# Performance work log

Hardware: AMD Instinct MI355X
Metric: run time of the kernel (lower is better)

The kernel has to match this reference:

```python
import jax, jax.numpy as jnp
import numpy as np

B, T, C, H = 2, 2048, 1024, 4
D = C // H
STRIDES = [1, 3, 7, 13]  # spiral_strides[:n_head]
SCALE = 1.0 / float(np.sqrt(D))


def _build_mask():
    """Static [H, T, T] bool mask: spiral positions intersected with causal.
    Replicates: positions = set((i+offset)%T for offset in range(-T//2, T//2, stride)),
    then keep only p <= i."""
    m = np.zeros((H, T, T), dtype=bool)
    i = np.arange(T)
    causal = (np.arange(T)[None, :] <= i[:, None])
    for h in range(H):
        s = STRIDES[h % len(STRIDES)]
        off = np.arange(-(T // 2), T // 2, s)
        pos = (i[:, None] + off[None, :]) % T  # [T, n_off]
        mh = np.zeros((T, T), dtype=bool)
        mh[np.repeat(i, len(off)), pos.ravel()] = True  # set semantics (dupes ok)
        m[h] = mh & causal
    return jnp.asarray(m)

MASK = _build_mask()  # [H, T, T]


def setup_inputs() -> dict:
    ks = jax.random.split(jax.random.key(0), 4)
    s = 0.02
    return {
        "x": jax.random.normal(ks[0], (B, T, C), jnp.float32),
        "Wqk": jax.random.normal(ks[1], (C, C), jnp.float32) * s,
        "bqk": jnp.zeros((C,), jnp.float32),
        "Wv": jax.random.normal(ks[2], (C, C), jnp.float32) * s,
        "bv": jnp.zeros((C,), jnp.float32),
        "Wo": jax.random.normal(ks[3], (C, C), jnp.float32) * s,
        "bo": jnp.zeros((C,), jnp.float32),
    }


def reference(x, Wqk, bqk, Wv, bv, Wo, bo):
    qk = x @ Wqk.T + bqk                                   # [B,T,C]; q == k in source
    q = qk.reshape(B, T, H, D).transpose(0, 2, 1, 3)       # [B,H,T,D]
    v = (x @ Wv.T + bv).reshape(B, T, H, D).transpose(0, 2, 1, 3)
    scores = jnp.einsum('bhid,bhjd->bhij', q, q) * SCALE   # [B,H,T,T]
    NEG = jnp.float32(-1e30)
    logits = jnp.where(MASK[None], scores, NEG)
    w = jax.nn.softmax(logits, axis=-1)
    # Rows with no causal spiral position stay all-zero (matches torch scatter behavior)
    w = jnp.where(MASK[None], w, jnp.float32(0.0))
    out = jnp.einsum('bhij,bhjd->bhid', w, v)              # [B,H,T,D]
    out = out.transpose(0, 2, 1, 3).reshape(B, T, C)
    return out @ Wo.T + bo
```

## Files before the change

### kernel.cpp

```cpp
#include <hip/hip_runtime.h>
#include <cstdint>
#include <cstddef>

typedef unsigned short u16;
typedef uint32_t u32;
typedef __bf16 bf16x8 __attribute__((ext_vector_type(8)));
typedef float f32x4 __attribute__((ext_vector_type(4)));
typedef float f32x16 __attribute__((ext_vector_type(16)));

typedef __attribute__((address_space(1))) void gvoid;
typedef __attribute__((address_space(3))) void lvoid;

__device__ __forceinline__ void g2l16(const void* g, void* l) {
    __builtin_amdgcn_global_load_lds((gvoid*)g, (lvoid*)l, 16, 0, 0);
}

__device__ __forceinline__ u16 f2bf(float f) {
    union { float f; uint32_t u; } v;
    v.f = f;
    uint32_t r = (v.u + 0x7FFFu + ((v.u >> 16) & 1u)) >> 16;
    return (u16)r;
}

__device__ const int T_h[24]  = {0, 1,1,1, 2,2,2,2,2,2,2, 3,3,3,3,3,3,3,3,3,3,3,3,3};
__device__ const int T_g[24]  = {0, 0,1,2, 0,1,2,3,4,5,6, 0,1,2,3,4,5,6,7,8,9,10,11,12};
__device__ const int T_qt[24] = {0, 64,86,108, 130,140,150,160,170,180,190,
                                 200,205,210,215,220,225,230,235,240,245,250,255,260};
__device__ const int T_LQ[24] = {2048, 683,683,682, 293,293,293,293,292,292,292,
                                 158,158,158,158,158,158,158,157,157,157,157,157,157};
__device__ const int T_ktB[24]= {0, 64,86,108, 140,150,160,170,180,190,130,
                                 245,250,255,260,200,205,210,215,220,225,230,235,240};
__device__ const int T_LkB[24]= {2048, 683,683,682, 293,293,293,292,292,292,293,
                                 157,157,157,157,158,158,158,158,158,158,158,157,157};
__device__ const int T_cB[24] = {1, -341,-341,-341, -146,-146,-146,-146,-146,-146,-145,
                                 -79,-79,-79,-79,-78,-78,-78,-78,-78,-78,-78,-78,-78};
__device__ const int T_ktA[24]= {0, 108,64,86, 180,190,130,140,150,160,170,
                                 215,220,225,230,235,240,245,250,255,260,200,205,210};
__device__ const int T_LkA[24]= {0, 682,683,683, 292,292,293,293,293,293,292,
                                 158,158,158,158,157,157,157,157,157,157,158,158,158};
__device__ const int T_cA[24] = {0, -342,-341,-341, -147,-147,-146,-146,-146,-146,-146,
                                 -79,-79,-79,-79,-79,-79,-79,-79,-79,-79,-78,-78,-78};
__device__ const int T_dA[24] = {0, 0,1,1, 0,0,1,1,1,1,1, 0,0,0,0,0,0,0,0,0,0,1,1,1};
__device__ const int T_nc[24] = {16, 6,6,6, 3,3,3,3,3,3,3, 2,2,2,2,2,2,2,2,2,2,2,2,2};

__device__ __forceinline__ void col_geom(int p, int c, int& ntB, int& tA0, int& nt) {
    const int LQ = T_LQ[p];
    const int Mc = c << 7;
    int mmax = Mc + 128; if (mmax > LQ) mmax = LQ; mmax -= 1;
    int jB = mmax + T_cB[p];
    if (jB < 0) jB = 0;
    if (jB > T_LkB[p]) jB = T_LkB[p];
    ntB = (jB + 31) >> 5;
    int jlo = Mc + T_cA[p]; if (jlo < 0) jlo = 0;
    int jhi = mmax + T_dA[p];
    if (jhi > T_LkA[p]) jhi = T_LkA[p];
    tA0 = jlo >> 5;
    int ntA = 0;
    if (jhi > jlo) ntA = ((jhi + 31) >> 5) - tA0;
    nt = ntB + ntA;
}

__device__ __forceinline__ u16* partO_addr(u16* lo, u16* hi, int slot) {
    return (slot < 128) ? (lo + (size_t)slot * 32768) : (hi + (size_t)(slot - 128) * 32768);
}
__device__ __forceinline__ const u16* partO_addr_c(const u16* lo, const u16* hi, int slot) {
    return (slot < 128) ? (lo + (size_t)slot * 32768) : (hi + (size_t)(slot - 128) * 32768);
}

__global__ __launch_bounds__(256)
void cvt_kernel(const float* __restrict__ x, const float* __restrict__ wqk,
                const float* __restrict__ wv, const float* __restrict__ wo,
                u16* __restrict__ out) {
    int i = (blockIdx.x * 256 + threadIdx.x) * 4;
    const float* src;
    int off;
    if (i < 4194304)      { src = x;   off = 0; }
    else if (i < 5242880) { src = wqk; off = 4194304; }
    else if (i < 6291456) { src = wv;  off = 5242880; }
    else                  { src = wo;  off = 6291456; }
    float4 v = *(const float4*)(src + (i - off));
    ushort4 o;
    o.x = f2bf(v.x); o.y = f2bf(v.y); o.z = f2bf(v.z); o.w = f2bf(v.w);
    *(ushort4*)(out + i) = o;
}

__global__ __launch_bounds__(256, 3)
void gemm_qkv(const u16* __restrict__ A, const u16* __restrict__ Bq, const u16* __restrict__ Bv,
              const float* __restrict__ bq, const float* __restrict__ bv,
              u16* __restrict__ qkb, u16* __restrict__ vb) {
    __shared__ __align__(16) u16 As[2][4096], Bqs[2][2048], Bvs[2][2048];
    const int bid = blockIdx.x;
    const int m0 = (bid >> 4) * 128;
    const int n0 = (bid & 15) * 64;
    const int t = threadIdx.x;
    const int lane = t & 63;
    const int wid = t >> 6;
    const int wr = wid >> 1, wc = wid & 1;
    const int l15 = lane & 15, l4 = lane >> 4;

    f32x4 aq[4][2] = {}, av[4][2] = {};

    auto stage = [&](int buf, int kt) {
        const int kbase = kt * 32;
#pragma unroll
        for (int c2 = 0; c2 < 2; ++c2) {
            const int pp = c2 * 4096 + t * 16;
            g2l16(A + (size_t)(m0 + (pp >> 6)) * 1024 + kbase + ((pp & 63) >> 1), (char*)As[buf] + pp);
        }
        const int pb = t * 16;
        const int rb = pb >> 6, kb = (pb & 63) >> 1;
        g2l16(Bq + (size_t)(n0 + rb) * 1024 + kbase + kb, (char*)Bqs[buf] + pb);
        g2l16(Bv + (size_t)(n0 + rb) * 1024 + kbase + kb, (char*)Bvs[buf] + pb);
    };

    stage(0, 0);
    asm volatile("s_waitcnt vmcnt(0)" ::: "memory");
    __syncthreads();

    int cur = 0;
    for (int kt = 0; kt < 32; ++kt) {
        if (kt + 1 < 32) stage(cur ^ 1, kt + 1);
        bf16x8 af[4], bfq[2], bfv[2];
#pragma unroll
        for (int mi = 0; mi < 4; ++mi)
            af[mi] = *(const bf16x8*)((const char*)As[cur] + (wr * 64 + mi * 16 + l15) * 64 + l4 * 16);
#pragma unroll
        for (int ni = 0; ni < 2; ++ni) {
            bfq[ni] = *(const bf16x8*)((const char*)Bqs[cur] + (wc * 32 + ni * 16 + l15) * 64 + l4 * 16);
            bfv[ni] = *(const bf16x8*)((const char*)Bvs[cur] + (wc * 32 + ni * 16 + l15) * 64 + l4 * 16);
        }
        __builtin_amdgcn_s_setprio(1);
#pragma unroll
        for (int mi = 0; mi < 4; ++mi)
#pragma unroll
            for (int ni = 0; ni < 2; ++ni) {
                aq[mi][ni] = __builtin_amdgcn_mfma_f32_16x16x32_bf16(af[mi], bfq[ni], aq[mi][ni], 0, 0, 0);
                av[mi][ni] = __builtin_amdgcn_mfma_f32_16x16x32_bf16(af[mi], bfv[ni], av[mi][ni], 0, 0, 0);
            }
        __builtin_amdgcn_s_setprio(0);
        asm volatile("s_waitcnt vmcnt(0)" ::: "memory");
        __syncthreads();
        cur ^= 1;
    }

    const int mbase = m0 + wr * 64 + l4 * 4;
    const int nbase = n0 + wc * 32 + l15;
#pragma unroll
    for (int ni = 0; ni < 2; ++ni) {
        const int n = nbase + ni * 16;
        const float bq_ = bq[n];
        const float bv_ = bv[n];
#pragma unroll
        for (int mi = 0; mi < 4; ++mi) {
            const int mrow = mbase + mi * 16;
#pragma unroll
            for (int r = 0; r < 4; ++r) {
                qkb[(size_t)(mrow + r) * 1024 + n] = f2bf(aq[mi][ni][r] + bq_);
                vb [(size_t)(mrow + r) * 1024 + n] = f2bf(av[mi][ni][r] + bv_);
            }
        }
    }
}

__device__ __forceinline__ void tile_decode(int tt, int& h, int& cls, int& jt, int& LK) {
    if (tt < 64)       { h = 0; cls = 0;               jt = tt;              LK = 2048; }
    else if (tt < 130) { h = 1; cls = (tt - 64) / 22;  jt = (tt - 64) % 22;  LK = (cls < 2) ? 683 : 682; }
    else if (tt < 200) { h = 2; cls = (tt - 130) / 10; jt = (tt - 130) % 10; LK = (cls < 4) ? 293 : 292; }
    else               { h = 3; cls = (tt - 200) / 5;  jt = (tt - 200) % 5;  LK = (cls < 7) ? 158 : 157; }
}

__global__ __launch_bounds__(256)
void repack_kv(const u16* __restrict__ qkb, const u16* __restrict__ vb,
               u16* __restrict__ kpack, u16* __restrict__ vpack) {
    __shared__ __align__(16) unsigned char sm[32768];
    const int bid = blockIdx.x;
    const int b = bid & 1;
    const int tt = bid >> 1;
    int h, cls, jt, LK;
    tile_decode(tt, h, cls, jt, LK);
    const int s = (h == 0) ? 1 : (h == 1) ? 3 : (h == 2) ? 7 : 13;
    const int j0 = jt * 32;
    int nval = LK - j0; if (nval > 32) nval = 32;
    const int t = threadIdx.x;

#pragma unroll
    for (int i2 = 0; i2 < 4; ++i2) {
        const int p = i2 * 4096 + t * 16;
        const int j = p >> 9;
        const int cb = (p & 511) ^ ((j & 31) << 4);
        const int jj = (j < nval) ? j : (nval - 1);
        const size_t gofs = (size_t)((b * 2048 + cls + (j0 + jj) * s) * 1024 + h * 256) + (cb >> 1);
        g2l16(qkb + gofs, sm + p);
        g2l16(vb  + gofs, sm + 16384 + p);
    }
    asm volatile("s_waitcnt vmcnt(0)" ::: "memory");
    __syncthreads();
    if (nval < 32) {
        const int pb = 16384 + nval * 512;
        for (int off = pb + t * 16; off < 32768; off += 4096) {
            uint4 z; z.x = 0; z.y = 0; z.z = 0; z.w = 0;
            *(uint4*)(sm + off) = z;
        }
        __syncthreads();
    }
    const size_t tb = (size_t)(b * 265 + tt) * 8192;
#pragma unroll
    for (int i2 = 0; i2 < 4; ++i2) {
        const int o = (i2 * 256 + t) * 8;
        const int dc = o >> 9;
        const int idx = (o >> 3) & 63;
        const int j = idx & 31;
        const int d0 = dc * 16 + (idx >> 5) * 8;
        const uint4 pk = *(const uint4*)(sm + j * 512 + ((d0 * 2) ^ ((j & 31) << 4)));
        *(uint4*)(kpack + tb + o) = pk;
    }
#pragma unroll
    for (int i2 = 0; i2 < 4; ++i2) {
        const int o = (i2 * 256 + t) * 8;
        const int slot2 = o >> 9;
        const int idx = (o >> 3) & 63;
        const int jb = (slot2 >> 3) * 16 + (idx >> 5) * 8;
        const int d = (slot2 & 7) * 32 + (idx & 31);
        u32 wpk[4];
#pragma unroll
        for (int e2 = 0; e2 < 4; ++e2) {
            const int j1 = jb + e2 * 2, j2 = j1 + 1;
            const u16 a0 = *(const u16*)(sm + 16384 + j1 * 512 + (((d >> 3) ^ (j1 & 31)) << 4) + (d & 7) * 2);
            const u16 a1 = *(const u16*)(sm + 16384 + j2 * 512 + (((d >> 3) ^ (j2 & 31)) << 4) + (d & 7) * 2);
            wpk[e2] = (u32)a0 | ((u32)a1 << 16);
        }
        uint4 pk; pk.x = wpk[0]; pk.y = wpk[1]; pk.z = wpk[2]; pk.w = wpk[3];
        *(uint4*)(vpack + tb + o) = pk;
    }
}

__global__ __launch_bounds__(256, 2)
void attn_kernel(const u16* __restrict__ kpack, const u16* __restrict__ vpack,
                 u16* __restrict__ attnb, u16* __restrict__ partLo, u16* __restrict__ partHi,
                 float* __restrict__ mlbuf) {
    __shared__ __align__(16) unsigned char sm[65536];
    static constexpr int CGc[24] = {0,16,22,28,34,37,40,43,46,49,52,55,
                                    57,59,61,63,65,67,69,71,73,75,77,79};
    static constexpr int EXc[24] = {0,56,64,72,80,82,84,86,88,90,92,94,
                                    94,94,94,94,94,94,94,94,94,94,94,94};
    static constexpr int Tpc[24] = {72,14,14,14,5,5,5,5,5,5,5,2,2,2,2,2,2,2,2,2,2,2,2,2};

    const int bid = blockIdx.x;
    const int xcd = bid & 7, slot = bid >> 3;
    const int b = xcd & 1, quad = xcd >> 1;
    int hsel, hcb;
    if (quad <= 1) {
        if (slot < 36)      { hsel = 0; hcb = quad * 36 + slot; }
        else if (slot < 49) { hsel = 3; hcb = quad * 13 + (slot - 36); }
        else return;
    } else if (quad == 2) {
        if (slot >= 42) return;
        hsel = 1; hcb = slot;
    } else {
        if (slot >= 35) return;
        hsel = 2; hcb = slot;
    }
    int p = (hsel == 0) ? 0 : (hsel == 1) ? 1 : (hsel == 2) ? 4 : 11;
    int rb = hcb;
    while (rb >= Tpc[p]) { rb -= Tpc[p]; ++p; }
    int colg = CGc[p], exb = EXc[p];

    const int LQ = T_LQ[p];
    const int cB = T_cB[p], cA = T_cA[p], dA = T_dA[p];
    const int LKB = T_LkB[p], LKA = T_LkA[p];
    const int ktB = T_ktB[p], ktA = T_ktA[p];
    const int h = T_h[p], g = T_g[p], nc = T_nc[p], qt0 = T_qt[p];
    const int s = (h == 0) ? 1 : (h == 1) ? 3 : (h == 2) ? 7 : 13;

    int col = 0, chunk = 0, ntB = 0, tA0 = 0, nt = 0;
    for (int c = nc - 1; c >= 0; --c) {
        const int Mc = c << 7;
        int mmax = Mc + 128; if (mmax > LQ) mmax = LQ; mmax -= 1;
        int jB = mmax + cB; if (jB < 0) jB = 0; if (jB > LKB) jB = LKB;
        const int nb = (jB + 31) >> 5;
        int jlo = Mc + cA; if (jlo < 0) jlo = 0;
        int jhi = mmax + dA; if (jhi > LKA) jhi = LKA;
        const int ta = jlo >> 5;
        const int na = (jhi > jlo) ? (((jhi + 31) >> 5) - ta) : 0;
        const int n = nb + na;
        const int nch2 = (n + 7) >> 3;
        if (rb < nch2) { col = c; chunk = rb; ntB = nb; tA0 = ta; nt = n; break; }
        rb -= nch2; ++colg; exb += nch2 - 1;
    }
    const int nch = (nt + 7) >> 3;
    const int PBi = b * 265;

    const int t = threadIdx.x;
    const int w = t >> 6;
    const int l = t & 63;
    const int l31 = l & 31, h5 = l >> 5;
    const int m = (col << 7) + (w << 5) + l31;
    const float c2 = 0.09016844f;
    const int lane16 = l * 16;

    bf16x8 qf[16];
    {
        const u16* qb = kpack + (size_t)(PBi + qt0 + col * 4 + w) * 8192 + l * 8;
#pragma unroll
        for (int dc = 0; dc < 16; ++dc)
            qf[dc] = *(const bf16x8*)(qb + dc * 512);
    }

    auto tileof = [&](int tv) -> int {
        return (tv < ntB) ? (ktB + tv) : (ktA + tA0 + (tv - ntB));
    };
    auto stage = [&](int tv, int buf) {
        const size_t tb = (size_t)(PBi + tileof(tv)) * 8192;
        unsigned char* Kd = sm + buf * 32768;
        unsigned char* Vd = Kd + 16384;
#pragma unroll
        for (int i2 = 0; i2 < 4; ++i2) {
            const int off = i2 * 4096 + t * 16;
            g2l16(kpack + tb + (off >> 1), Kd + off);
            g2l16(vpack + tb + (off >> 1), Vd + off);
        }
    };

    const int tt0 = chunk * 8;
    int tt1 = tt0 + 8; if (tt1 > nt) tt1 = nt;

    f32x16 o[8] = {};
    float mrun = -3.0e38f, lrun = 0.0f;

    stage(tt0, 0);
    asm volatile("s_waitcnt vmcnt(0)" ::: "memory");
    __syncthreads();

    int buf = 0;
    for (int tv = tt0; tv < tt1; ++tv) {
        if (tv + 1 < tt1) stage(tv + 1, buf ^ 1);

        int j0, lo, hi;
        if (tv < ntB) { j0 = tv << 5; lo = -100000; hi = cB; }
        else { const int ta = tA0 + tv - ntB; j0 = ta << 5; lo = cA; hi = dA; }

        const unsigned char* Kb = sm + buf * 32768;
        const unsigned char* Vb = Kb + 16384;

        f32x16 sacc = {};
        __builtin_amdgcn_s_setprio(1);
#pragma unroll
        for (int dc = 0; dc < 16; ++dc) {
            const bf16x8 kf = *(const bf16x8*)(Kb + dc * 1024 + lane16);
            sacc = __builtin_amdgcn_mfma_f32_32x32x16_bf16(kf, qf[dc], sacc, 0, 0, 0);
        }
        __builtin_amdgcn_s_setprio(0);

        const int ebase = j0 - m;
        float tmax = -3.0e38f;
#pragma unroll
        for (int r = 0; r < 16; ++r) {
            const int km = (r & 3) + 8 * (r >> 2) + 4 * h5;
            const int e = ebase + km;
            const bool ok = (e >= lo) && (e < hi);
            sacc[r] = ok ? sacc[r] : -3.0e38f;
            tmax = fmaxf(tmax, sacc[r]);
        }
        tmax = fmaxf(tmax, __shfl_xor(tmax, 32, 64));
        if (!__all(tmax <= mrun + 8.0f)) {
            const float mnew = fmaxf(mrun, tmax);
            const float fsc = __builtin_amdgcn_exp2f((mrun - mnew) * c2);
            lrun *= fsc;
#pragma unroll
            for (int ch = 0; ch < 8; ++ch)
#pragma unroll
                for (int r = 0; r < 16; ++r)
                    o[ch][r] *= fsc;
            mrun = mnew;
        }
        float psum = 0.0f;
#pragma unroll
        for (int r = 0; r < 16; ++r) {
            const float pv = (sacc[r] > -1.0e37f) ? __builtin_amdgcn_exp2f((sacc[r] - mrun) * c2) : 0.0f;
            sacc[r] = pv;
            psum += pv;
        }
        lrun += psum;

        uint32_t w0, w1, w2, w3, w4, w5, w6, w7;
        asm("v_cvt_pk_bf16_f32 %0,%1,%2" : "=v"(w0) : "v"(sacc[0]),  "v"(sacc[1]));
        asm("v_cvt_pk_bf16_f32 %0,%1,%2" : "=v"(w1) : "v"(sacc[2]),  "v"(sacc[3]));
        asm("v_cvt_pk_bf16_f32 %0,%1,%2" : "=v"(w2) : "v"(sacc[4]),  "v"(sacc[5]));
        asm("v_cvt_pk_bf16_f32 %0,%1,%2" : "=v"(w3) : "v"(sacc[6]),  "v"(sacc[7]));
        asm("v_cvt_pk_bf16_f32 %0,%1,%2" : "=v"(w4) : "v"(sacc[8]),  "v"(sacc[9]));
        asm("v_cvt_pk_bf16_f32 %0,%1,%2" : "=v"(w5) : "v"(sacc[10]), "v"(sacc[11]));
        asm("v_cvt_pk_bf16_f32 %0,%1,%2" : "=v"(w6) : "v"(sacc[12]), "v"(sacc[13]));
        asm("v_cvt_pk_bf16_f32 %0,%1,%2" : "=v"(w7) : "v"(sacc[14]), "v"(sacc[15]));
        asm("v_permlane32_swap_b32 %0, %1" : "+v"(w0), "+v"(w2));
        asm("v_permlane32_swap_b32 %0, %1" : "+v"(w1), "+v"(w3));
        asm("v_permlane32_swap_b32 %0, %1" : "+v"(w4), "+v"(w6));
        asm("v_permlane32_swap_b32 %0, %1" : "+v"(w5), "+v"(w7));
        union { uint32_t u[4]; bf16x8 v; } p0u, p1u;
        p0u.u[0] = w0; p0u.u[1] = w1; p0u.u[2] = w2; p0u.u[3] = w3;
        p1u.u[0] = w4; p1u.u[1] = w5; p1u.u[2] = w6; p1u.u[3] = w7;

        __builtin_amdgcn_s_setprio(1);
#pragma unroll
        for (int kk = 0; kk < 2; ++kk) {
            const bf16x8 pf = kk ? p1u.v : p0u.v;
#pragma unroll
            for (int ch = 0; ch < 8; ++ch) {
                const bf16x8 vf = *(const bf16x8*)(Vb + (kk * 8 + ch) * 1024 + lane16);
                o[ch] = __builtin_amdgcn_mfma_f32_32x32x16_bf16(vf, pf, o[ch], 0, 0, 0);
            }
        }
        __builtin_amdgcn_s_setprio(0);

        asm volatile("s_waitcnt vmcnt(0)" ::: "memory");
        __syncthreads();
        buf ^= 1;
    }

    lrun += __shfl_xor(lrun, 32, 64);

    float scale = 1.0f;
    u16* ab;
    const int qm = (w << 5) + l31;
    if (nch == 1) {
        scale = (lrun > 0.0f) ? 1.0f / lrun : 0.0f;
        ab = attnb + ((size_t)(b * 2048 + g + m * s)) * 1024 + h * 256;
    } else {
        if (h5 == 0 && m < LQ) {
            const int colid = b * 81 + colg;
            mlbuf[(size_t)((colid * 8 + chunk) * 256) + qm * 2]     = mrun;
            mlbuf[(size_t)((colid * 8 + chunk) * 256) + qm * 2 + 1] = lrun;
        }
        if (chunk == 0)
            ab = attnb + ((size_t)(b * 2048 + g + m * s)) * 1024 + h * 256;
        else
            ab = partO_addr(partLo, partHi, b * 94 + exb + chunk - 1) + (size_t)qm * 256;
    }

    if (m < LQ) {
#pragma unroll
        for (int ch = 0; ch < 8; ++ch) {
#pragma unroll
            for (int g2 = 0; g2 < 4; ++g2) {
                ushort4 wv4;
                wv4.x = f2bf(o[ch][g2 * 4 + 0] * scale);
                wv4.y = f2bf(o[ch][g2 * 4 + 1] * scale);
                wv4.z = f2bf(o[ch][g2 * 4 + 2] * scale);
                wv4.w = f2bf(o[ch][g2 * 4 + 3] * scale);
                *(ushort4*)(ab + ch * 32 + 8 * g2 + 4 * h5) = wv4;
            }
        }
    }
}

__global__ __launch_bounds__(256)
void combine_kernel(const u16* __restrict__ partLo, const u16* __restrict__ partHi,
                    const float* __restrict__ mlbuf, u16* __restrict__ attnb) {
    static constexpr int MCc[24] = {0,14,18,22,26,28,30,32,34,36,38,40,
                                    40,40,40,40,40,40,40,40,40,40,40,40};
    static constexpr int CGc[24] = {0,16,22,28,34,37,40,43,46,49,52,55,
                                    57,59,61,63,65,67,69,71,73,75,77,79};
    static constexpr int EXc[24] = {0,56,64,72,80,82,84,86,88,90,92,94,
                                    94,94,94,94,94,94,94,94,94,94,94,94};
    const int b = blockIdx.x & 1;
    int rb = blockIdx.x >> 1;
    int p = 0, base = 0, colg = 0, exb = 0;
#pragma unroll
    for (int i = 1; i < 24; ++i)
        if (rb >= MCc[i]) { p = i; base = MCc[i]; colg = CGc[i]; exb = EXc[i]; }
    rb -= base;

    int col = 0, nch = 0;
    for (int c = T_nc[p] - 1; c >= 0; --c) {
        int nb, ta, n;
        col_geom(p, c, nb, ta, n);
        const int nc2 = (n + 7) >> 3;
        if (nc2 > 1) {
            if (rb == 0) { col = c; nch = nc2; break; }
            --rb;
        }
        ++colg; exb += nc2 - 1;
    }
    const int h = T_h[p], g = T_g[p];
    const int s = (h == 0) ? 1 : (h == 1) ? 3 : (h == 2) ? 7 : 13;
    const int LQ = T_LQ[p];
    const int colid = b * 81 + colg;
    const float c2 = 0.09016844f;

    const int t = threadIdx.x;
    const int q = t >> 1, dpart = (t & 1) * 128;
    const int m = (col << 7) + q;

    float mj[8], lj[8];
#pragma unroll
    for (int j5 = 0; j5 < 8; ++j5) {
        if (j5 < nch) {
            mj[j5] = mlbuf[(size_t)((colid * 8 + j5) * 256) + q * 2];
            lj[j5] = mlbuf[(size_t)((colid * 8 + j5) * 256) + q * 2 + 1];
        } else { mj[j5] = -3.0e38f; lj[j5] = 0.0f; }
    }
    float M = -3.0e38f;
#pragma unroll
    for (int j5 = 0; j5 < 8; ++j5) if (j5 < nch) M = fmaxf(M, mj[j5]);
    float L = 0.0f, al[8];
#pragma unroll
    for (int j5 = 0; j5 < 8; ++j5) {
        al[j5] = (j5 < nch) ? __builtin_amdgcn_exp2f((mj[j5] - M) * c2) : 0.0f;
        L += lj[j5] * al[j5];
    }
    const float inv = (L > 0.0f) ? 1.0f / L : 0.0f;
#pragma unroll
    for (int j5 = 0; j5 < 8; ++j5) al[j5] *= inv;

    u16* dst = attnb + ((size_t)(b * 2048 + g + m * s)) * 1024 + h * 256 + dpart;

    for (int ss = 0; ss < 4; ++ss) {
        float acc32[32];
#pragma unroll
        for (int e = 0; e < 32; ++e) acc32[e] = 0.0f;
#pragma unroll
        for (int j5 = 0; j5 < 8; ++j5) {
            if (j5 >= nch) continue;
            const u16* src = (j5 == 0)
                ? (dst + ss * 32)
                : (partO_addr_c(partLo, partHi, b * 94 + exb + j5 - 1) + (size_t)q * 256 + dpart + ss * 32);
            const float sc = al[j5];
#pragma unroll
            for (int w4 = 0; w4 < 4; ++w4) {
                const uint4 pk = *(const uint4*)(src + w4 * 8);
                const u32 ww[4] = { pk.x, pk.y, pk.z, pk.w };
#pragma unroll
                for (int e = 0; e < 4; ++e) {
                    union { u32 u; float f; } lo2, hi2;
                    lo2.u = ww[e] << 16;
                    hi2.u = ww[e] & 0xffff0000u;
                    acc32[w4 * 8 + e * 2]     += sc * lo2.f;
                    acc32[w4 * 8 + e * 2 + 1] += sc * hi2.f;
                }
            }
        }
        if (m < LQ) {
#pragma unroll
            for (int w4 = 0; w4 < 4; ++w4) {
                uint4 pk;
                pk.x = (u32)f2bf(acc32[w4 * 8 + 0]) | ((u32)f2bf(acc32[w4 * 8 + 1]) << 16);
                pk.y = (u32)f2bf(acc32[w4 * 8 + 2]) | ((u32)f2bf(acc32[w4 * 8 + 3]) << 16);
                pk.z = (u32)f2bf(acc32[w4 * 8 + 4]) | ((u32)f2bf(acc32[w4 * 8 + 5]) << 16);
                pk.w = (u32)f2bf(acc32[w4 * 8 + 6]) | ((u32)f2bf(acc32[w4 * 8 + 7]) << 16);
                *(uint4*)(dst + ss * 32 + w4 * 8) = pk;
            }
        }
    }
}

__global__ __launch_bounds__(256, 3)
void gemm_out(const u16* __restrict__ A, const u16* __restrict__ Bw,
              const float* __restrict__ bias, float* __restrict__ outp) {
    __shared__ __align__(16) u16 As[2][4096], Bs[2][2048];
    const int bid = blockIdx.x;
    const int m0 = (bid >> 4) * 128;
    const int n0 = (bid & 15) * 64;
    const int t = threadIdx.x;
    const int lane = t & 63;
    const int wid = t >> 6;
    const int wr = wid >> 1, wc = wid & 1;
    const int l15 = lane & 15, l4 = lane >> 4;

    f32x4 acc[4][2] = {};

    auto stage = [&](int buf, int kt) {
        const int kbase = kt * 32;
#pragma unroll
        for (int c2 = 0; c2 < 2; ++c2) {
            const int pp = c2 * 4096 + t * 16;
            g2l16(A + (size_t)(m0 + (pp >> 6)) * 1024 + kbase + ((pp & 63) >> 1), (char*)As[buf] + pp);
        }
        const int pb = t * 16;
        g2l16(Bw + (size_t)(n0 + (pb >> 6)) * 1024 + kbase + ((pb & 63) >> 1), (char*)Bs[buf] + pb);
    };

    stage(0, 0);
    asm volatile("s_waitcnt vmcnt(0)" ::: "memory");
    __syncthreads();

    int cur = 0;
    for (int kt = 0; kt < 32; ++kt) {
        if (kt + 1 < 32) stage(cur ^ 1, kt + 1);
        bf16x8 af[4], bfr[2];
#pragma unroll
        for (int mi = 0; mi < 4; ++mi)
            af[mi] = *(const bf16x8*)((const char*)As[cur] + (wr * 64 + mi * 16 + l15) * 64 + l4 * 16);
#pragma unroll
        for (int ni = 0; ni < 2; ++ni)
            bfr[ni] = *(const bf16x8*)((const char*)Bs[cur] + (wc * 32 + ni * 16 + l15) * 64 + l4 * 16);
        __builtin_amdgcn_s_setprio(1);
#pragma unroll
        for (int mi = 0; mi < 4; ++mi)
#pragma unroll
            for (int ni = 0; ni < 2; ++ni)
                acc[mi][ni] = __builtin_amdgcn_mfma_f32_16x16x32_bf16(af[mi], bfr[ni], acc[mi][ni], 0, 0, 0);
        __builtin_amdgcn_s_setprio(0);
        asm volatile("s_waitcnt vmcnt(0)" ::: "memory");
        __syncthreads();
        cur ^= 1;
    }

    const int mbase = m0 + wr * 64 + l4 * 4;
    const int nbase = n0 + wc * 32 + l15;
#pragma unroll
    for (int ni = 0; ni < 2; ++ni) {
        const int n = nbase + ni * 16;
        const float bv = bias[n];
#pragma unroll
        for (int mi = 0; mi < 4; ++mi) {
            const int mrow = mbase + mi * 16;
#pragma unroll
            for (int r = 0; r < 4; ++r)
                outp[(size_t)(mrow + r) * 1024 + n] = acc[mi][ni][r] + bv;
        }
    }
}

extern "C" void kernel_launch(void* const* d_in, const int* in_sizes, int n_in,
                              void* d_out, int out_size, void* d_ws, size_t ws_size,
                              hipStream_t stream) {
    const float* x   = (const float*)d_in[0];
    const float* Wqk = (const float*)d_in[1];
    const float* bqk = (const float*)d_in[2];
    const float* Wv  = (const float*)d_in[3];
    const float* bv  = (const float*)d_in[4];
    const float* Wo  = (const float*)d_in[5];
    const float* bo  = (const float*)d_in[6];
    float* out = (float*)d_out;

    u16* ws     = (u16*)d_ws;
    u16* xb     = ws;
    u16* wqkb   = ws + 4194304;
    u16* wvb    = ws + 5242880;
    u16* wob    = ws + 6291456;
    u16* qkb    = ws + 7340032;
    u16* vb     = ws + 11534336;
    u16* kpack  = ws + 15728640;
    u16* vpack  = ws + 20070400;
    u16* attnb  = ws;
    u16* partLo = ws + 7340032;
    u16* partHi = ws + 4194304;
    float* mlbuf = (float*)d_out;

    cvt_kernel<<<7168, 256, 0, stream>>>(x, Wqk, Wv, Wo, ws);
    gemm_qkv<<<512, 256, 0, stream>>>(xb, wqkb, wvb, bqk, bv, qkb, vb);
    repack_kv<<<530, 256, 0, stream>>>(qkb, vb, kpack, vpack);
    attn_kernel<<<392, 256, 0, stream>>>(kpack, vpack, attnb, partLo, partHi, mlbuf);
    combine_kernel<<<80, 256, 0, stream>>>(partLo, partHi, mlbuf, attnb);
    gemm_out<<<512, 256, 0, stream>>>(attnb, wob, bo, out);
}
```

Baseline: 123.5 us.

## Fuse K/V repacking into QKV GEMM epilogue, removing repack kernel

```diff
diff --git a/kernel.cpp b/kernel.cpp
--- a/kernel.cpp
+++ b/kernel.cpp
@@ -87,7 +87,7 @@
 __global__ __launch_bounds__(256, 3)
 void gemm_qkv(const u16* __restrict__ A, const u16* __restrict__ Bq, const u16* __restrict__ Bv,
               const float* __restrict__ bq, const float* __restrict__ bv,
-              u16* __restrict__ qkb, u16* __restrict__ vb) {
+              u16* __restrict__ kpack, u16* __restrict__ vpack) {
     __shared__ __align__(16) u16 As[2][4096], Bqs[2][2048], Bvs[2][2048];
     const int bid = blockIdx.x;
     const int m0 = (bid >> 4) * 128;
@@ -143,94 +143,113 @@
         cur ^= 1;
     }
 
+    const int tm0 = m0 & 2047;
+    const int b_  = m0 >> 11;
+    const int hh  = n0 >> 8;
+    const int dd0 = n0 & 255;
+    const int sS  = (hh == 0) ? 1 : (hh == 1) ? 3 : (hh == 2) ? 7 : 13;
+    const int cb0 = (hh == 0) ? 0 : (hh == 1) ? 64 : (hh == 2) ? 130 : 200;
+    const int cbs = (hh == 0) ? 1 : (hh == 1) ? 22 : (hh == 2) ? 10 : 5;
+    const size_t PB = (size_t)b_ * 265 * 8192;
+    u16* lds = &As[0][0];
     const int mbase = m0 + wr * 64 + l4 * 4;
     const int nbase = n0 + wc * 32 + l15;
+    const bool padfill = (tm0 == 1920);
+
 #pragma unroll
     for (int ni = 0; ni < 2; ++ni) {
         const int n = nbase + ni * 16;
+        const int dloc2 = (n - n0) * 2;
         const float bq_ = bq[n];
+#pragma unroll
+        for (int mi = 0; mi < 4; ++mi)
+#pragma unroll
+            for (int r = 0; r < 4; ++r) {
+                const int row = mbase + mi * 16 + r - m0;
+                *(u16*)((char*)lds + row * 128 + (dloc2 ^ ((row & 7) << 4))) = f2bf(aq[mi][ni][r] + bq_);
+            }
+    }
+    __syncthreads();
+    {
+        const int jK = t & 31;
+        const int dof = (t >> 5) * 16;
+        const int dK = dd0 + (t >> 5) * 8;
+        const int destoff = (dK >> 4) * 512 + (((t >> 5) & 1) * 32 + jK) * 8;
+        for (int cls = 0; cls < sS; ++cls) {
+            const int jf = (tm0 - cls + sS - 1) / sS;
+            const int jl = (tm0 + 127 - cls) / sS;
+            const int baseT = cb0 + cbs * cls;
+            for (int jt = jf >> 5; jt <= (jl >> 5); ++jt) {
+                const int j = (jt << 5) + jK;
+                if (j >= jf && j <= jl) {
+                    const int row = cls + j * sS - tm0;
+                    const bf16x8 v = *(const bf16x8*)((char*)lds + row * 128 + (dof ^ ((row & 7) << 4)));
+                    *(bf16x8*)(kpack + PB + (size_t)(baseT + jt) * 8192 + destoff) = v;
+                }
+            }
+        }
+    }
+    __syncthreads();
+
+#pragma unroll
+    for (int ni = 0; ni < 2; ++ni) {
+        const int n = nbase + ni * 16;
+        const int dloc2 = (n - n0) * 2;
         const float bv_ = bv[n];
 #pragma unroll
-        for (int mi = 0; mi < 4; ++mi) {
-            const int mrow = mbase + mi * 16;
+        for (int mi = 0; mi < 4; ++mi)
 #pragma unroll
             for (int r = 0; r < 4; ++r) {
-                qkb[(size_t)(mrow + r) * 1024 + n] = f2bf(aq[mi][ni][r] + bq_);
-                vb [(size_t)(mrow + r) * 1024 + n] = f2bf(av[mi][ni][r] + bv_);
-            }
-        }
-    }
-}
-
-__device__ __forceinline__ void tile_decode(int tt, int& h, int& cls, int& jt, int& LK) {
-    if (tt < 64)       { h = 0; cls = 0;               jt = tt;              LK = 2048; }
-    else if (tt < 130) { h = 1; cls = (tt - 64) / 22;  jt = (tt - 64) % 22;  LK = (cls < 2) ? 683 : 682; }
-    else if (tt < 200) { h = 2; cls = (tt - 130) / 10; jt = (tt - 130) % 10; LK = (cls < 4) ? 293 : 292; }
-    else               { h = 3; cls = (tt - 200) / 5;  jt = (tt - 200) % 5;  LK = (cls < 7) ? 158 : 157; }
-}
-
-__global__ __launch_bounds__(256)
-void repack_kv(const u16* __restrict__ qkb, const u16* __restrict__ vb,
-               u16* __restrict__ kpack, u16* __restrict__ vpack) {
-    __shared__ __align__(16) unsigned char sm[32768];
-    const int bid = blockIdx.x;
-    const int b = bid & 1;
-    const int tt = bid >> 1;
-    int h, cls, jt, LK;
-    tile_decode(tt, h, cls, jt, LK);
-    const int s = (h == 0) ? 1 : (h == 1) ? 3 : (h == 2) ? 7 : 13;
-    const int j0 = jt * 32;
-    int nval = LK - j0; if (nval > 32) nval = 32;
-    const int t = threadIdx.x;
-
-#pragma unroll
-    for (int i2 = 0; i2 < 4; ++i2) {
-        const int p = i2 * 4096 + t * 16;
-        const int j = p >> 9;
-        const int cb = (p & 511) ^ ((j & 31) << 4);
-        const int jj = (j < nval) ? j : (nval - 1);
-        const size_t gofs = (size_t)((b * 2048 + cls + (j0 + jj) * s) * 1024 + h * 256) + (cb >> 1);
-        g2l16(qkb + gofs, sm + p);
-        g2l16(vb  + gofs, sm + 16384 + p);
-    }
-    asm volatile("s_waitcnt vmcnt(0)" ::: "memory");
+                const int row = mbase + mi * 16 + r - m0;
+                *(u16*)((char*)lds + row * 128 + (dloc2 ^ ((row & 7) << 4))) = f2bf(av[mi][ni][r] + bv_);
+            }
+    }
     __syncthreads();
-    if (nval < 32) {
-        const int pb = 16384 + nval * 512;
-        for (int off = pb + t * 16; off < 32768; off += 4096) {
-            uint4 z; z.x = 0; z.y = 0; z.z = 0; z.w = 0;
-            *(uint4*)(sm + off) = z;
-        }
-        __syncthreads();
-    }
-    const size_t tb = (size_t)(b * 265 + tt) * 8192;
-#pragma unroll
-    for (int i2 = 0; i2 < 4; ++i2) {
-        const int o = (i2 * 256 + t) * 8;
-        const int dc = o >> 9;
-        const int idx = (o >> 3) & 63;
-        const int j = idx & 31;
-        const int d0 = dc * 16 + (idx >> 5) * 8;
-        const uint4 pk = *(const uint4*)(sm + j * 512 + ((d0 * 2) ^ ((j & 31) << 4)));
-        *(uint4*)(kpack + tb + o) = pk;
-    }
-#pragma unroll
-    for (int i2 = 0; i2 < 4; ++i2) {
-        const int o = (i2 * 256 + t) * 8;
-        const int slot2 = o >> 9;
-        const int idx = (o >> 3) & 63;
-        const int jb = (slot2 >> 3) * 16 + (idx >> 5) * 8;
-        const int d = (slot2 & 7) * 32 + (idx & 31);
-        u32 wpk[4];
-#pragma unroll
-        for (int e2 = 0; e2 < 4; ++e2) {
-            const int j1 = jb + e2 * 2, j2 = j1 + 1;
-            const u16 a0 = *(const u16*)(sm + 16384 + j1 * 512 + (((d >> 3) ^ (j1 & 31)) << 4) + (d & 7) * 2);
-            const u16 a1 = *(const u16*)(sm + 16384 + j2 * 512 + (((d >> 3) ^ (j2 & 31)) << 4) + (d & 7) * 2);
-            wpk[e2] = (u32)a0 | ((u32)a1 << 16);
-        }
-        uint4 pk; pk.x = wpk[0]; pk.y = wpk[1]; pk.z = wpk[2]; pk.w = wpk[3];
-        *(uint4*)(vpack + tb + o) = pk;
+    {
+        const int dV = dd0 + (t & 63);
+        const int jg = t >> 6;
+        const int dloc2 = (t & 63) * 2;
+        const int destoff = ((jg >> 1) * 8 + (dV >> 5)) * 512 + ((jg & 1) * 32 + (dV & 31)) * 8;
+        auto ldv = [&](int row) -> u16 {
+            return *(const u16*)((char*)lds + row * 128 + (dloc2 ^ ((row & 7) << 4)));
+        };
+        for (int cls = 0; cls < sS; ++cls) {
+            const int jf = (tm0 - cls + sS - 1) / sS;
+            const int jl = (tm0 + 127 - cls) / sS;
+            const int baseT = cb0 + cbs * cls;
+            for (int jt = jf >> 5; jt <= (jl >> 5); ++jt) {
+                const int jb = (jt << 5) + jg * 8;
+                int e0 = jf - jb; if (e0 < 0) e0 = 0;
+                int ev = jl - jb; if (ev > 7) ev = 7;
+                int e1w = ev;
+                if (padfill && jt == (jl >> 5)) e1w = 7;
+                if (e0 > e1w) continue;
+                const int rowb = cls + jb * sS - tm0;
+                u16* dst = vpack + PB + (size_t)(baseT + jt) * 8192 + destoff;
+                if (e0 == 0 && e1w == 7) {
+                    const u16 a0 = (0 <= ev) ? ldv(rowb)          : (u16)0;
+                    const u16 a1 = (1 <= ev) ? ldv(rowb + sS)     : (u16)0;
+                    const u16 a2 = (2 <= ev) ? ldv(rowb + 2 * sS) : (u16)0;
+                    const u16 a3 = (3 <= ev) ? ldv(rowb + 3 * sS) : (u16)0;
+                    const u16 a4 = (4 <= ev) ? ldv(rowb + 4 * sS) : (u16)0;
+                    const u16 a5 = (5 <= ev) ? ldv(rowb + 5 * sS) : (u16)0;
+                    const u16 a6 = (6 <= ev) ? ldv(rowb + 6 * sS) : (u16)0;
+                    const u16 a7 = (7 <= ev) ? ldv(rowb + 7 * sS) : (u16)0;
+                    uint4 pk;
+                    pk.x = (u32)a0 | ((u32)a1 << 16);
+                    pk.y = (u32)a2 | ((u32)a3 << 16);
+                    pk.z = (u32)a4 | ((u32)a5 << 16);
+                    pk.w = (u32)a6 | ((u32)a7 << 16);
+                    *(uint4*)dst = pk;
+                } else {
+#pragma unroll
+                    for (int e = 0; e < 8; ++e) {
+                        if (e >= e0 && e <= e1w)
+                            dst[e] = (e <= ev) ? ldv(rowb + e * sS) : (u16)0;
+                    }
+                }
+            }
+        }
     }
 }
 
@@ -637,8 +656,6 @@
     u16* wqkb   = ws + 4194304;
     u16* wvb    = ws + 5242880;
     u16* wob    = ws + 6291456;
-    u16* qkb    = ws + 7340032;
-    u16* vb     = ws + 11534336;
     u16* kpack  = ws + 15728640;
     u16* vpack  = ws + 20070400;
     u16* attnb  = ws;
@@ -647,8 +664,7 @@
     float* mlbuf = (float*)d_out;
 
     cvt_kernel<<<7168, 256, 0, stream>>>(x, Wqk, Wv, Wo, ws);
-    gemm_qkv<<<512, 256, 0, stream>>>(xb, wqkb, wvb, bqk, bv, qkb, vb);
-    repack_kv<<<530, 256, 0, stream>>>(qkb, vb, kpack, vpack);
+    gemm_qkv<<<512, 256, 0, stream>>>(xb, wqkb, wvb, bqk, bv, kpack, vpack);
     attn_kernel<<<392, 256, 0, stream>>>(kpack, vpack, attnb, partLo, partHi, mlbuf);
     combine_kernel<<<80, 256, 0, stream>>>(partLo, partHi, mlbuf, attnb);
     gemm_out<<<512, 256, 0, stream>>>(attnb, wob, bo, out);
```

New measurement: 131.6 us. 6.5% more time.
